# Kernel optimization log

Measured on AMD Instinct MI355X. Metric: run time of the kernel, lower is better.

The kernel has to match this reference:

```python
import jax, jax.numpy as jnp
import numpy as np

B, L, IN_DIM, D_MODEL, N_LAYERS = 4, 1024, 64, 512, 3
D_INNER, STATE, DT_RANK, K = 1024, 16, 32, 4  # expand=2, dt_rank=d_model//16, conv kernel 4


def setup_inputs() -> dict:
    key = jax.random.key(0)
    ks = jax.random.split(key, 8)
    s = 0.02
    def rn(k, shp):
        return jax.random.normal(k, shp, jnp.float32) * s
    inp = {"x": jax.random.normal(ks[0], (B, L, IN_DIM), jnp.float32)}
    inp["input_w"] = rn(ks[1], (D_MODEL, IN_DIM)); inp["input_b"] = jnp.zeros((D_MODEL,), jnp.float32)
    inp["in_proj_w"] = rn(ks[2], (N_LAYERS, 2 * D_INNER, D_MODEL)); inp["in_proj_b"] = jnp.zeros((N_LAYERS, 2 * D_INNER), jnp.float32)
    inp["conv_w"] = rn(ks[3], (N_LAYERS, D_INNER, 1, K)); inp["conv_b"] = jnp.zeros((N_LAYERS, D_INNER), jnp.float32)
    inp["x_proj_w"] = rn(ks[4], (N_LAYERS, DT_RANK + 2 * STATE, D_INNER))
    inp["dt_proj_w"] = rn(ks[5], (N_LAYERS, D_INNER, DT_RANK)); inp["dt_proj_b"] = jnp.full((N_LAYERS, D_INNER), -4.0, jnp.float32)
    inp["A_log"] = jnp.tile(jnp.log(jnp.arange(1, STATE + 1, dtype=jnp.float32))[None, None, :], (N_LAYERS, D_INNER, 1))
    inp["D"] = jnp.ones((N_LAYERS, D_INNER), jnp.float32)
    inp["out_proj_w"] = rn(ks[6], (N_LAYERS, D_MODEL, D_INNER)); inp["out_proj_b"] = jnp.zeros((N_LAYERS, D_MODEL), jnp.float32)
    inp["ln_w"] = jnp.ones((N_LAYERS, D_MODEL), jnp.float32); inp["ln_b"] = jnp.zeros((N_LAYERS, D_MODEL), jnp.float32)
    return inp


def _layernorm(x, w, b):
    mu = jnp.mean(x, -1, keepdims=True)
    v = jnp.var(x, -1, keepdims=True)
    return (x - mu) * jax.lax.rsqrt(v + 1e-5) * w + b


def _mamba(u, iw, ib, cw, cb, xw, dw, db, A_log, Dp, ow, ob):
    # u: [B, L, d_model]
    xz = u @ iw.T + ib                          # [B, L, 2*d_inner]
    xp, z = jnp.split(xz, 2, axis=-1)
    # causal depthwise conv over time
    xc = jax.lax.conv_general_dilated(xp.transpose(0, 2, 1), cw, (1,), [(K - 1, 0)],
                                      feature_group_count=D_INNER,
                                      dimension_numbers=("NCH", "OIH", "NCH")) + cb[None, :, None]
    xc = jax.nn.silu(xc).transpose(0, 2, 1)     # [B, L, d_inner]
    proj = xc @ xw.T                            # [B, L, dt_rank + 2*N]
    dtl = proj[..., :DT_RANK]
    Bm = proj[..., DT_RANK:DT_RANK + STATE]
    Cm = proj[..., DT_RANK + STATE:]
    dt = jax.nn.softplus(dtl @ dw.T + db)       # [B, L, d_inner]
    A = -jnp.exp(A_log)                         # [d_inner, N]

    def step(h, t):
        dt_t, B_t, C_t, x_t = t                 # [B,d], [B,N], [B,N], [B,d]
        h = h * jnp.exp(dt_t[..., None] * A) + (dt_t * x_t)[..., None] * B_t[:, None, :]
        return h, jnp.einsum("bdn,bn->bd", h, C_t)

    h0 = jnp.zeros((u.shape[0], D_INNER, STATE), u.dtype)
    _, ys = jax.lax.scan(step, h0, (dt.transpose(1, 0, 2), Bm.transpose(1, 0, 2),
                                    Cm.transpose(1, 0, 2), xc.transpose(1, 0, 2)))
    y = ys.transpose(1, 0, 2) + xc * Dp
    y = y * jax.nn.silu(z)
    return y @ ow.T + ob


def reference(x, input_w, input_b, in_proj_w, in_proj_b, conv_w, conv_b, x_proj_w,
              dt_proj_w, dt_proj_b, A_log, D, out_proj_w, out_proj_b, ln_w, ln_b):
    h = x @ input_w.T + input_b                 # [B, L, d_model]
    for i in range(N_LAYERS):
        res = h
        h = _mamba(h, in_proj_w[i], in_proj_b[i], conv_w[i], conv_b[i], x_proj_w[i],
                   dt_proj_w[i], dt_proj_b[i], A_log[i], D[i], out_proj_w[i], out_proj_b[i])
        h = _layernorm(h + res, ln_w[i], ln_b[i])
    return h[:, -1, :]
```

## Files before the change

kernel.cpp:

```cpp
#include <hip/hip_runtime.h>
#include <hip/hip_bf16.h>
#include <cstddef>
#include <cstdint>

#define NB 4
#define NL 1024
#define IN_DIM 64
#define D_MODEL 512
#define N_LAYERS 3
#define D_INNER 1024
#define NSTATE 16
#define DT_RANK 32
#define KCONV 4
#define NROWS (NB * NL)
#define CHUNK 16
#define NCHUNK (NL / CHUNK)
#define LOG2E 1.4426950408889634f

typedef __attribute__((ext_vector_type(8))) short short8;
typedef __attribute__((ext_vector_type(4))) float f32x4;
typedef __attribute__((ext_vector_type(4))) unsigned short us4;
typedef unsigned short ushort_t;

__device__ __forceinline__ ushort_t f2b1(float x) {
  uint32_t u = __builtin_bit_cast(uint32_t, x);
  u += 0x7fffu + ((u >> 16) & 1u);
  return (ushort_t)(u >> 16);
}
__device__ __forceinline__ float b2f(ushort_t u) {
  return __builtin_bit_cast(float, (uint32_t)u << 16);
}

__device__ __forceinline__ void gload_lds16(const ushort_t* src, short* dst) {
  __builtin_amdgcn_global_load_lds(
      (const __attribute__((address_space(1))) uint32_t*)src,
      (__attribute__((address_space(3))) uint32_t*)dst, 16, 0, 0);
}

#define E0 (NROWS * IN_DIM)
#define E1 (D_MODEL * IN_DIM)
#define E2 (N_LAYERS * 2 * D_INNER * D_MODEL)
#define E3 (N_LAYERS * 64 * D_INNER)
#define E4 (N_LAYERS * D_INNER * DT_RANK)
#define E5 (N_LAYERS * D_MODEL * D_INNER)
#define ETOT (E0 + E1 + E2 + E3 + E4 + E5)

__global__ __launch_bounds__(256) void cvt_all(
    const float* __restrict__ x, const float* __restrict__ inw,
    const float* __restrict__ ipw, const float* __restrict__ xpw,
    const float* __restrict__ dpw, const float* __restrict__ opw,
    ushort_t* __restrict__ xb, ushort_t* __restrict__ inwb,
    ushort_t* __restrict__ iwb, ushort_t* __restrict__ xwb,
    ushort_t* __restrict__ dwb, ushort_t* __restrict__ owb)
{
  int i = (blockIdx.x * 256 + threadIdx.x) * 4;
  if (i >= ETOT) return;
  const float* src; ushort_t* dst; int off;
  if      (i < E0)                  { src = x;   dst = xb;   off = i; }
  else if (i < E0+E1)               { src = inw; dst = inwb; off = i - E0; }
  else if (i < E0+E1+E2)            { src = ipw; dst = iwb;  off = i - (E0+E1); }
  else if (i < E0+E1+E2+E3)         { src = xpw; dst = xwb;  off = i - (E0+E1+E2); }
  else if (i < E0+E1+E2+E3+E4)      { src = dpw; dst = dwb;  off = i - (E0+E1+E2+E3); }
  else                              { src = opw; dst = owb;  off = i - (E0+E1+E2+E3+E4); }
  const float4 v = *(const float4*)(src + off);
  us4 o;
  o.x = f2b1(v.x); o.y = f2b1(v.y); o.z = f2b1(v.z); o.w = f2b1(v.w);
  *(us4*)(dst + off) = o;
}

template<int BM, int BN, int MF, int NF, int ACT, bool WF32, bool WB16>
__global__ __launch_bounds__(256) void gemm_mfma(
    const ushort_t* __restrict__ A, int lda,
    const ushort_t* __restrict__ W,
    const float* __restrict__ bias,
    float* __restrict__ Cf, ushort_t* __restrict__ Cb,
    int M, int N, int K)
{
  constexpr int CA = BM / 64;
  constexpr int CB = BN / 64;
  __shared__ __align__(16) short sa[BM * 32];
  __shared__ __align__(16) short sb[BN * 32];

  const int tid = threadIdx.x;
  const int l = tid & 63;
  const int wid = tid >> 6;
  const int wrow = (wid >> 1) * (BM / 2);
  const int wcol = (wid & 1) * (BN / 2);
  const int m0 = blockIdx.y * BM;
  const int n0 = blockIdx.x * BN;

  const int srow = l >> 2;
  const int scol = (l & 3) * 8;

  f32x4 acc[MF][NF] = {};

  for (int k0 = 0; k0 < K; k0 += 32) {
#pragma unroll
    for (int c = 0; c < CA; ++c) {
      short* dst = sa + (c * 4 + wid) * 512;
      const ushort_t* src =
          A + (size_t)(m0 + (c * 4 + wid) * 16 + srow) * lda + k0 + scol;
      gload_lds16(src, dst);
    }
#pragma unroll
    for (int c = 0; c < CB; ++c) {
      short* dst = sb + (c * 4 + wid) * 512;
      const ushort_t* src =
          W + (size_t)(n0 + (c * 4 + wid) * 16 + srow) * K + k0 + scol;
      gload_lds16(src, dst);
    }
    __syncthreads();

    short8 af[MF], bfr[NF];
#pragma unroll
    for (int mi = 0; mi < MF; ++mi)
      af[mi] = *(const short8*)(sa + (wrow + mi * 16 + (l & 15)) * 32 + (l >> 4) * 8);
#pragma unroll
    for (int nj = 0; nj < NF; ++nj)
      bfr[nj] = *(const short8*)(sb + (wcol + nj * 16 + (l & 15)) * 32 + (l >> 4) * 8);
#pragma unroll
    for (int mi = 0; mi < MF; ++mi)
#pragma unroll
      for (int nj = 0; nj < NF; ++nj)
        acc[mi][nj] = __builtin_amdgcn_mfma_f32_16x16x32_bf16(
            af[mi], bfr[nj], acc[mi][nj], 0, 0, 0);
    __syncthreads();
  }

#pragma unroll
  for (int nj = 0; nj < NF; ++nj) {
    const int col = n0 + wcol + nj * 16 + (l & 15);
    const float bv = bias ? bias[col] : 0.f;
#pragma unroll
    for (int mi = 0; mi < MF; ++mi) {
#pragma unroll
      for (int q = 0; q < 4; ++q) {
        const int row = m0 + wrow + mi * 16 + (l >> 4) * 4 + q;
        float v = acc[mi][nj][q] + bv;
        if (ACT == 1) v = (v > 20.f) ? v : log1pf(__expf(v));
        if (WF32) Cf[(size_t)row * N + col] = v;
        if (WB16) Cb[(size_t)row * N + col] = f2b1(v);
      }
    }
  }
}

__global__ __launch_bounds__(256) void conv_silu(
    const ushort_t* __restrict__ xzb,
    const float* __restrict__ cw,
    const float* __restrict__ cb,
    ushort_t* __restrict__ xcb)
{
  const int idx = blockIdx.x * 256 + threadIdx.x;
  const int d4 = (idx & (D_INNER / 4 - 1)) * 4;
  const int bt = idx >> 8;
  const int t = bt & (NL - 1);
  const int b = bt >> 10;

  float acc4[4];
  {
    const float4 cbv = *(const float4*)(cb + d4);
    acc4[0] = cbv.x; acc4[1] = cbv.y; acc4[2] = cbv.z; acc4[3] = cbv.w;
  }
  float wv[4][4];
#pragma unroll
  for (int i = 0; i < 4; ++i) {
    const float4 w = *(const float4*)(cw + (size_t)(d4 + i) * KCONV);
    wv[i][0] = w.x; wv[i][1] = w.y; wv[i][2] = w.z; wv[i][3] = w.w;
  }
#pragma unroll
  for (int j = 0; j < KCONV; ++j) {
    const int tt = t - (KCONV - 1) + j;
    if (tt >= 0) {
      const us4 xv = *(const us4*)(xzb + (size_t)(b * NL + tt) * (2 * D_INNER) + d4);
      acc4[0] = fmaf(b2f(xv.x), wv[0][j], acc4[0]);
      acc4[1] = fmaf(b2f(xv.y), wv[1][j], acc4[1]);
      acc4[2] = fmaf(b2f(xv.z), wv[2][j], acc4[2]);
      acc4[3] = fmaf(b2f(xv.w), wv[3][j], acc4[3]);
    }
  }
  us4 o;
#pragma unroll
  for (int i = 0; i < 4; ++i) {
    const float s = acc4[i] / (1.f + __expf(-acc4[i]));
    ((ushort_t*)&o)[i] = f2b1(s);
  }
  *(us4*)(xcb + (size_t)idx * 4) = o;
}

__global__ __launch_bounds__(256) void scan_phase1(
    const ushort_t* __restrict__ dtb,
    const float* __restrict__ proj,
    const ushort_t* __restrict__ xcb,
    const float* __restrict__ A_log,
    float* __restrict__ S_loc,
    float* __restrict__ sumdt)
{
  __shared__ float prs[CHUNK][64];
  const int d = blockIdx.x * 256 + threadIdx.x;
  const int c = blockIdx.y;
  const int b = blockIdx.z;
  const int t0 = c * CHUNK;

#pragma unroll
  for (int i = 0; i < 4; ++i) {
    const int idx = i * 256 + threadIdx.x;
    prs[idx >> 6][idx & 63] =
        proj[((size_t)(b * NL + t0) + (idx >> 6)) * 64 + (idx & 63)];
  }
  __syncthreads();

  float A2[NSTATE];
#pragma unroll
  for (int n = 0; n < NSTATE; ++n)
    A2[n] = -__expf(A_log[d * NSTATE + n]) * LOG2E;

  float h[NSTATE];
#pragma unroll
  for (int n = 0; n < NSTATE; ++n) h[n] = 0.f;
  float sdt = 0.f;

#pragma unroll 4
  for (int tt = 0; tt < CHUNK; ++tt) {
    const size_t row = (size_t)(b * NL + t0 + tt);
    const float dtv = b2f(dtb[row * D_INNER + d]);
    const float xv = b2f(xcb[row * D_INNER + d]);
    float Bv[NSTATE];
    *(float4*)(Bv)      = *(const float4*)(&prs[tt][32]);
    *(float4*)(Bv + 4)  = *(const float4*)(&prs[tt][36]);
    *(float4*)(Bv + 8)  = *(const float4*)(&prs[tt][40]);
    *(float4*)(Bv + 12) = *(const float4*)(&prs[tt][44]);
    sdt += dtv;
    const float dx = dtv * xv;
#pragma unroll
    for (int n = 0; n < NSTATE; ++n)
      h[n] = fmaf(h[n], exp2f(dtv * A2[n]), dx * Bv[n]);
  }

  const size_t cbase = (size_t)(b * NCHUNK + c);
  sumdt[cbase * D_INNER + d] = sdt;
#pragma unroll
  for (int n = 0; n < NSTATE; ++n)
    S_loc[(cbase * NSTATE + n) * D_INNER + d] = h[n];
}

__global__ __launch_bounds__(256) void scan_carry(
    const float* __restrict__ S_loc,
    const float* __restrict__ sumdt,
    const float* __restrict__ A_log,
    float* __restrict__ H_in)
{
  const int idx = blockIdx.x * 256 + threadIdx.x;
  const int d = idx & (D_INNER - 1);
  const int n = (idx >> 10) & (NSTATE - 1);
  const int b = idx >> 14;

  const float A2n = -__expf(A_log[d * NSTATE + n]) * LOG2E;

  float H = 0.f;
  for (int c = 0; c < NCHUNK; ++c) {
    const size_t cbase = (size_t)(b * NCHUNK + c);
    H_in[(cbase * NSTATE + n) * D_INNER + d] = H;
    const float sdt = sumdt[cbase * D_INNER + d];
    H = fmaf(H, exp2f(A2n * sdt), S_loc[(cbase * NSTATE + n) * D_INNER + d]);
  }
}

__global__ __launch_bounds__(256) void scan_phase2(
    const ushort_t* __restrict__ dtb,
    const float* __restrict__ proj,
    const ushort_t* __restrict__ xcb,
    const ushort_t* __restrict__ xzb,
    const float* __restrict__ A_log,
    const float* __restrict__ Dp,
    const float* __restrict__ H_in,
    ushort_t* __restrict__ yb)
{
  __shared__ float prs[CHUNK][64];
  const int d = blockIdx.x * 256 + threadIdx.x;
  const int c = blockIdx.y;
  const int b = blockIdx.z;
  const int t0 = c * CHUNK;

#pragma unroll
  for (int i = 0; i < 4; ++i) {
    const int idx = i * 256 + threadIdx.x;
    prs[idx >> 6][idx & 63] =
        proj[((size_t)(b * NL + t0) + (idx >> 6)) * 64 + (idx & 63)];
  }
  __syncthreads();

  float A2[NSTATE];
#pragma unroll
  for (int n = 0; n < NSTATE; ++n)
    A2[n] = -__expf(A_log[d * NSTATE + n]) * LOG2E;

  const size_t cbase = (size_t)(b * NCHUNK + c);
  float h[NSTATE];
#pragma unroll
  for (int n = 0; n < NSTATE; ++n)
    h[n] = H_in[(cbase * NSTATE + n) * D_INNER + d];

  const float Dv = Dp[d];

#pragma unroll 4
  for (int tt = 0; tt < CHUNK; ++tt) {
    const size_t row = (size_t)(b * NL + t0 + tt);
    const size_t rd = row * D_INNER + d;
    const float dtv = b2f(dtb[rd]);
    const float xv = b2f(xcb[rd]);
    float Bv[NSTATE], Cv[NSTATE];
    *(float4*)(Bv)      = *(const float4*)(&prs[tt][32]);
    *(float4*)(Bv + 4)  = *(const float4*)(&prs[tt][36]);
    *(float4*)(Bv + 8)  = *(const float4*)(&prs[tt][40]);
    *(float4*)(Bv + 12) = *(const float4*)(&prs[tt][44]);
    *(float4*)(Cv)      = *(const float4*)(&prs[tt][48]);
    *(float4*)(Cv + 4)  = *(const float4*)(&prs[tt][52]);
    *(float4*)(Cv + 8)  = *(const float4*)(&prs[tt][56]);
    *(float4*)(Cv + 12) = *(const float4*)(&prs[tt][60]);
    const float dx = dtv * xv;
    float accv = 0.f;
#pragma unroll
    for (int n = 0; n < NSTATE; ++n) {
      h[n] = fmaf(h[n], exp2f(dtv * A2[n]), dx * Bv[n]);
      accv = fmaf(h[n], Cv[n], accv);
    }
    const float zv = b2f(xzb[row * (2 * D_INNER) + D_INNER + d]);
    float yv = fmaf(xv, Dv, accv);
    yv *= zv / (1.f + __expf(-zv));
    yb[rd] = f2b1(yv);
  }
}

__global__ __launch_bounds__(256) void add_ln(
    const float* __restrict__ x,
    const float* __restrict__ res,
    const float* __restrict__ w,
    const float* __restrict__ bln,
    float* __restrict__ out,
    ushort_t* __restrict__ outb,
    float* __restrict__ out2)
{
  const int wave = threadIdx.x >> 6;
  const int lane = threadIdx.x & 63;
  const int row = blockIdx.x * 4 + wave;
  const float* xr = x + (size_t)row * D_MODEL;
  const float* rr = res + (size_t)row * D_MODEL;

  float v[8];
  float s = 0.f, s2 = 0.f;
#pragma unroll
  for (int i = 0; i < 8; ++i) {
    const float t = xr[lane + i * 64] + rr[lane + i * 64];
    v[i] = t; s += t; s2 = fmaf(t, t, s2);
  }
#pragma unroll
  for (int off = 32; off; off >>= 1) {
    s += __shfl_xor(s, off);
    s2 += __shfl_xor(s2, off);
  }
  const float mean = s * (1.f / D_MODEL);
  const float var = s2 * (1.f / D_MODEL) - mean * mean;
  const float rstd = rsqrtf(var + 1e-5f);
  const bool last_t = (row & (NL - 1)) == (NL - 1);
#pragma unroll
  for (int i = 0; i < 8; ++i) {
    const int c = lane + i * 64;
    const float o = (v[i] - mean) * rstd * w[c] + bln[c];
    out[(size_t)row * D_MODEL + c] = o;
    outb[(size_t)row * D_MODEL + c] = f2b1(o);
    if (out2 && last_t) out2[(size_t)(row >> 10) * D_MODEL + c] = o;
  }
}

extern "C" void kernel_launch(void* const* d_in, const int* in_sizes, int n_in,
                              void* d_out, int out_size, void* d_ws, size_t ws_size,
                              hipStream_t stream)
{
  const float* x         = (const float*)d_in[0];
  const float* input_w   = (const float*)d_in[1];
  const float* input_b   = (const float*)d_in[2];
  const float* in_proj_w = (const float*)d_in[3];
  const float* in_proj_b = (const float*)d_in[4];
  const float* conv_w    = (const float*)d_in[5];
  const float* conv_b    = (const float*)d_in[6];
  const float* x_proj_w  = (const float*)d_in[7];
  const float* dt_proj_w = (const float*)d_in[8];
  const float* dt_proj_b = (const float*)d_in[9];
  const float* A_log     = (const float*)d_in[10];
  const float* Dp        = (const float*)d_in[11];
  const float* out_proj_w= (const float*)d_in[12];
  const float* out_proj_b= (const float*)d_in[13];
  const float* ln_w      = (const float*)d_in[14];
  const float* ln_b      = (const float*)d_in[15];

  float* p = (float*)d_ws;
  float* h0   = p; p += (size_t)NROWS * D_MODEL;
  float* h1   = p; p += (size_t)NROWS * D_MODEL;
  float* tmp  = p; p += (size_t)NROWS * D_MODEL;
  float* proj = p; p += (size_t)NROWS * 64;
  float* Sloc = p; p += (size_t)NB * NCHUNK * NSTATE * D_INNER;
  float* Hin  = p; p += (size_t)NB * NCHUNK * NSTATE * D_INNER;
  float* sdt  = p; p += (size_t)NB * NCHUNK * D_INNER;
  ushort_t* q = (ushort_t*)p;
  ushort_t* xzb   = q; q += (size_t)NROWS * 2 * D_INNER;
  ushort_t* xcb   = q; q += (size_t)NROWS * D_INNER;
  ushort_t* dtbb  = q; q += (size_t)NROWS * D_INNER;
  ushort_t* projb = q; q += (size_t)NROWS * 64;
  ushort_t* yb    = q; q += (size_t)NROWS * D_INNER;
  ushort_t* hb    = q; q += (size_t)NROWS * D_MODEL;
  ushort_t* xb    = q; q += (size_t)E0;
  ushort_t* inwb  = q; q += (size_t)E1;
  ushort_t* iwb   = q; q += (size_t)E2;
  ushort_t* xwb   = q; q += (size_t)E3;
  ushort_t* dwb   = q; q += (size_t)E4;
  ushort_t* owb   = q; q += (size_t)E5;

  cvt_all<<<(ETOT / 4 + 255) / 256, 256, 0, stream>>>(
      x, input_w, in_proj_w, x_proj_w, dt_proj_w, out_proj_w,
      xb, inwb, iwb, xwb, dwb, owb);

  gemm_mfma<64, 64, 2, 2, 0, true, true>
      <<<dim3(D_MODEL / 64, NROWS / 64), 256, 0, stream>>>(
      xb, IN_DIM, inwb, input_b, h0, hb, NROWS, D_MODEL, IN_DIM);

  float* hc = h0;
  float* hn = h1;

  for (int l = 0; l < N_LAYERS; ++l) {
    const ushort_t* iw = iwb + (size_t)l * 2 * D_INNER * D_MODEL;
    const float* ib = in_proj_b + (size_t)l * 2 * D_INNER;
    const float* cw = conv_w    + (size_t)l * D_INNER * KCONV;
    const float* cb = conv_b    + (size_t)l * D_INNER;
    const ushort_t* xw = xwb + (size_t)l * 64 * D_INNER;
    const ushort_t* dw = dwb + (size_t)l * D_INNER * DT_RANK;
    const float* db = dt_proj_b + (size_t)l * D_INNER;
    const float* Al = A_log     + (size_t)l * D_INNER * NSTATE;
    const float* Dl = Dp        + (size_t)l * D_INNER;
    const ushort_t* ow = owb + (size_t)l * D_MODEL * D_INNER;
    const float* ob = out_proj_b+ (size_t)l * D_MODEL;
    const float* lw = ln_w      + (size_t)l * D_MODEL;
    const float* lb = ln_b      + (size_t)l * D_MODEL;

    gemm_mfma<128, 128, 4, 4, 0, false, true>
        <<<dim3(2 * D_INNER / 128, NROWS / 128), 256, 0, stream>>>(
        hb, D_MODEL, iw, ib, nullptr, xzb, NROWS, 2 * D_INNER, D_MODEL);

    conv_silu<<<NROWS * D_INNER / 4 / 256, 256, 0, stream>>>(xzb, cw, cb, xcb);

    gemm_mfma<64, 64, 2, 2, 0, true, true>
        <<<dim3(1, NROWS / 64), 256, 0, stream>>>(
        xcb, D_INNER, xw, nullptr, proj, projb, NROWS, 64, D_INNER);

    gemm_mfma<128, 128, 4, 4, 1, false, true>
        <<<dim3(D_INNER / 128, NROWS / 128), 256, 0, stream>>>(
        projb, 64, dw, db, nullptr, dtbb, NROWS, D_INNER, DT_RANK);

    scan_phase1<<<dim3(D_INNER / 256, NCHUNK, NB), 256, 0, stream>>>(
        dtbb, proj, xcb, Al, Sloc, sdt);
    scan_carry<<<(NB * NSTATE * D_INNER) / 256, 256, 0, stream>>>(
        Sloc, sdt, Al, Hin);
    scan_phase2<<<dim3(D_INNER / 256, NCHUNK, NB), 256, 0, stream>>>(
        dtbb, proj, xcb, xzb, Al, Dl, Hin, yb);

    gemm_mfma<128, 128, 4, 4, 0, true, false>
        <<<dim3(D_MODEL / 128, NROWS / 128), 256, 0, stream>>>(
        yb, D_INNER, ow, ob, tmp, nullptr, NROWS, D_MODEL, D_INNER);

    add_ln<<<NROWS / 4, 256, 0, stream>>>(
        tmp, hc, lw, lb, hn, hb,
        (l == N_LAYERS - 1) ? (float*)d_out : nullptr);

    float* t2 = hc; hc = hn; hn = t2;
  }
}
```

Before: 600.3 us.

## Fuse dt projection and softplus into scan kernels, drop dt GEMM

Removes the separate dt_proj GEMM and its bf16 dt buffer. Each scan thread now loads its fp32 dt_proj weight row and computes dt by a 32-term dot product plus softplus from the projection already staged in shared memory. This cuts a kernel launch and the write and double read of a large intermediate, but adds per-timestep ALU work and register pressure in both scan phases. The out_proj GEMM tile is also changed to 64x128 to get more blocks.

```diff
diff --git a/kernel.cpp b/kernel.cpp
--- a/kernel.cpp
+++ b/kernel.cpp
@@ -41,34 +41,32 @@
 #define E1 (D_MODEL * IN_DIM)
 #define E2 (N_LAYERS * 2 * D_INNER * D_MODEL)
 #define E3 (N_LAYERS * 64 * D_INNER)
-#define E4 (N_LAYERS * D_INNER * DT_RANK)
 #define E5 (N_LAYERS * D_MODEL * D_INNER)
-#define ETOT (E0 + E1 + E2 + E3 + E4 + E5)
+#define ETOT (E0 + E1 + E2 + E3 + E5)
 
 __global__ __launch_bounds__(256) void cvt_all(
     const float* __restrict__ x, const float* __restrict__ inw,
     const float* __restrict__ ipw, const float* __restrict__ xpw,
-    const float* __restrict__ dpw, const float* __restrict__ opw,
+    const float* __restrict__ opw,
     ushort_t* __restrict__ xb, ushort_t* __restrict__ inwb,
     ushort_t* __restrict__ iwb, ushort_t* __restrict__ xwb,
-    ushort_t* __restrict__ dwb, ushort_t* __restrict__ owb)
+    ushort_t* __restrict__ owb)
 {
   int i = (blockIdx.x * 256 + threadIdx.x) * 4;
   if (i >= ETOT) return;
   const float* src; ushort_t* dst; int off;
-  if      (i < E0)                  { src = x;   dst = xb;   off = i; }
-  else if (i < E0+E1)               { src = inw; dst = inwb; off = i - E0; }
-  else if (i < E0+E1+E2)            { src = ipw; dst = iwb;  off = i - (E0+E1); }
-  else if (i < E0+E1+E2+E3)         { src = xpw; dst = xwb;  off = i - (E0+E1+E2); }
-  else if (i < E0+E1+E2+E3+E4)      { src = dpw; dst = dwb;  off = i - (E0+E1+E2+E3); }
-  else                              { src = opw; dst = owb;  off = i - (E0+E1+E2+E3+E4); }
+  if      (i < E0)            { src = x;   dst = xb;   off = i; }
+  else if (i < E0+E1)         { src = inw; dst = inwb; off = i - E0; }
+  else if (i < E0+E1+E2)      { src = ipw; dst = iwb;  off = i - (E0+E1); }
+  else if (i < E0+E1+E2+E3)   { src = xpw; dst = xwb;  off = i - (E0+E1+E2); }
+  else                        { src = opw; dst = owb;  off = i - (E0+E1+E2+E3); }
   const float4 v = *(const float4*)(src + off);
   us4 o;
   o.x = f2b1(v.x); o.y = f2b1(v.y); o.z = f2b1(v.z); o.w = f2b1(v.w);
   *(us4*)(dst + off) = o;
 }
 
-template<int BM, int BN, int MF, int NF, int ACT, bool WF32, bool WB16>
+template<int BM, int BN, int MF, int NF, bool WF32, bool WB16>
 __global__ __launch_bounds__(256) void gemm_mfma(
     const ushort_t* __restrict__ A, int lda,
     const ushort_t* __restrict__ W,
@@ -137,7 +135,6 @@
       for (int q = 0; q < 4; ++q) {
         const int row = m0 + wrow + mi * 16 + (l >> 4) * 4 + q;
         float v = acc[mi][nj][q] + bv;
-        if (ACT == 1) v = (v > 20.f) ? v : log1pf(__expf(v));
         if (WF32) Cf[(size_t)row * N + col] = v;
         if (WB16) Cb[(size_t)row * N + col] = f2b1(v);
       }
@@ -188,11 +185,31 @@
   *(us4*)(xcb + (size_t)idx * 4) = o;
 }
 
+__device__ __forceinline__ void load_dw_row(
+    const float* __restrict__ dpw, int d, float* dwr, float& dbv,
+    const float* __restrict__ db)
+{
+#pragma unroll
+  for (int i = 0; i < 8; ++i)
+    *(float4*)(dwr + i * 4) = *(const float4*)(dpw + (size_t)d * DT_RANK + i * 4);
+  dbv = db[d];
+}
+
+__device__ __forceinline__ float dt_fused(
+    const float* __restrict__ dtl, const float* __restrict__ dwr, float dbv)
+{
+  float a = dbv;
+#pragma unroll
+  for (int j = 0; j < DT_RANK; ++j) a = fmaf(dtl[j], dwr[j], a);
+  return (a > 20.f) ? a : log1pf(__expf(a));
+}
+
 __global__ __launch_bounds__(256) void scan_phase1(
-    const ushort_t* __restrict__ dtb,
     const float* __restrict__ proj,
     const ushort_t* __restrict__ xcb,
     const float* __restrict__ A_log,
+    const float* __restrict__ dpw,
+    const float* __restrict__ db,
     float* __restrict__ S_loc,
     float* __restrict__ sumdt)
 {
@@ -210,6 +227,9 @@
   }
   __syncthreads();
 
+  float dwr[DT_RANK]; float dbv;
+  load_dw_row(dpw, d, dwr, dbv, db);
+
   float A2[NSTATE];
 #pragma unroll
   for (int n = 0; n < NSTATE; ++n)
@@ -220,10 +240,9 @@
   for (int n = 0; n < NSTATE; ++n) h[n] = 0.f;
   float sdt = 0.f;
 
-#pragma unroll 4
   for (int tt = 0; tt < CHUNK; ++tt) {
     const size_t row = (size_t)(b * NL + t0 + tt);
-    const float dtv = b2f(dtb[row * D_INNER + d]);
+    const float dtv = dt_fused(&prs[tt][0], dwr, dbv);
     const float xv = b2f(xcb[row * D_INNER + d]);
     float Bv[NSTATE];
     *(float4*)(Bv)      = *(const float4*)(&prs[tt][32]);
@@ -267,11 +286,12 @@
 }
 
 __global__ __launch_bounds__(256) void scan_phase2(
-    const ushort_t* __restrict__ dtb,
     const float* __restrict__ proj,
     const ushort_t* __restrict__ xcb,
     const ushort_t* __restrict__ xzb,
     const float* __restrict__ A_log,
+    const float* __restrict__ dpw,
+    const float* __restrict__ db,
     const float* __restrict__ Dp,
     const float* __restrict__ H_in,
     ushort_t* __restrict__ yb)
@@ -290,6 +310,9 @@
   }
   __syncthreads();
 
+  float dwr[DT_RANK]; float dbv;
+  load_dw_row(dpw, d, dwr, dbv, db);
+
   float A2[NSTATE];
 #pragma unroll
   for (int n = 0; n < NSTATE; ++n)
@@ -303,11 +326,10 @@
 
   const float Dv = Dp[d];
 
-#pragma unroll 4
   for (int tt = 0; tt < CHUNK; ++tt) {
     const size_t row = (size_t)(b * NL + t0 + tt);
     const size_t rd = row * D_INNER + d;
-    const float dtv = b2f(dtb[rd]);
+    const float dtv = dt_fused(&prs[tt][0], dwr, dbv);
     const float xv = b2f(xcb[rd]);
     float Bv[NSTATE], Cv[NSTATE];
     *(float4*)(Bv)      = *(const float4*)(&prs[tt][32]);
@@ -405,22 +427,19 @@
   ushort_t* q = (ushort_t*)p;
   ushort_t* xzb   = q; q += (size_t)NROWS * 2 * D_INNER;
   ushort_t* xcb   = q; q += (size_t)NROWS * D_INNER;
-  ushort_t* dtbb  = q; q += (size_t)NROWS * D_INNER;
-  ushort_t* projb = q; q += (size_t)NROWS * 64;
   ushort_t* yb    = q; q += (size_t)NROWS * D_INNER;
   ushort_t* hb    = q; q += (size_t)NROWS * D_MODEL;
   ushort_t* xb    = q; q += (size_t)E0;
   ushort_t* inwb  = q; q += (size_t)E1;
   ushort_t* iwb   = q; q += (size_t)E2;
   ushort_t* xwb   = q; q += (size_t)E3;
-  ushort_t* dwb   = q; q += (size_t)E4;
   ushort_t* owb   = q; q += (size_t)E5;
 
   cvt_all<<<(ETOT / 4 + 255) / 256, 256, 0, stream>>>(
-      x, input_w, in_proj_w, x_proj_w, dt_proj_w, out_proj_w,
-      xb, inwb, iwb, xwb, dwb, owb);
-
-  gemm_mfma<64, 64, 2, 2, 0, true, true>
+      x, input_w, in_proj_w, x_proj_w, out_proj_w,
+      xb, inwb, iwb, xwb, owb);
+
+  gemm_mfma<64, 64, 2, 2, true, true>
       <<<dim3(D_MODEL / 64, NROWS / 64), 256, 0, stream>>>(
       xb, IN_DIM, inwb, input_b, h0, hb, NROWS, D_MODEL, IN_DIM);
 
@@ -433,7 +452,7 @@
     const float* cw = conv_w    + (size_t)l * D_INNER * KCONV;
     const float* cb = conv_b    + (size_t)l * D_INNER;
     const ushort_t* xw = xwb + (size_t)l * 64 * D_INNER;
-    const ushort_t* dw = dwb + (size_t)l * D_INNER * DT_RANK;
+    const float* dwf = dt_proj_w + (size_t)l * D_INNER * DT_RANK;
     const float* db = dt_proj_b + (size_t)l * D_INNER;
     const float* Al = A_log     + (size_t)l * D_INNER * NSTATE;
     const float* Dl = Dp        + (size_t)l * D_INNER;
@@ -442,29 +461,25 @@
     const float* lw = ln_w      + (size_t)l * D_MODEL;
     const float* lb = ln_b      + (size_t)l * D_MODEL;
 
-    gemm_mfma<128, 128, 4, 4, 0, false, true>
+    gemm_mfma<128, 128, 4, 4, false, true>
         <<<dim3(2 * D_INNER / 128, NROWS / 128), 256, 0, stream>>>(
         hb, D_MODEL, iw, ib, nullptr, xzb, NROWS, 2 * D_INNER, D_MODEL);
 
     conv_silu<<<NROWS * D_INNER / 4 / 256, 256, 0, stream>>>(xzb, cw, cb, xcb);
 
-    gemm_mfma<64, 64, 2, 2, 0, true, true>
+    gemm_mfma<64, 64, 2, 2, true, false>
         <<<dim3(1, NROWS / 64), 256, 0, stream>>>(
-        xcb, D_INNER, xw, nullptr, proj, projb, NROWS, 64, D_INNER);
-
-    gemm_mfma<128, 128, 4, 4, 1, false, true>
-        <<<dim3(D_INNER / 128, NROWS / 128), 256, 0, stream>>>(
-        projb, 64, dw, db, nullptr, dtbb, NROWS, D_INNER, DT_RANK);
+        xcb, D_INNER, xw, nullptr, proj, nullptr, NROWS, 64, D_INNER);
 
     scan_phase1<<<dim3(D_INNER / 256, NCHUNK, NB), 256, 0, stream>>>(
-        dtbb, proj, xcb, Al, Sloc, sdt);
+        proj, xcb, Al, dwf, db, Sloc, sdt);
     scan_carry<<<(NB * NSTATE * D_INNER) / 256, 256, 0, stream>>>(
         Sloc, sdt, Al, Hin);
     scan_phase2<<<dim3(D_INNER / 256, NCHUNK, NB), 256, 0, stream>>>(
-        dtbb, proj, xcb, xzb, Al, Dl, Hin, yb);
-
-    gemm_mfma<128, 128, 4, 4, 0, true, false>
-        <<<dim3(D_MODEL / 128, NROWS / 128), 256, 0, stream>>>(
+        proj, xcb, xzb, Al, dwf, db, Dl, Hin, yb);
+
+    gemm_mfma<64, 128, 2, 4, true, false>
+        <<<dim3(D_MODEL / 128, NROWS / 64), 256, 0, stream>>>(
         yb, D_INNER, ow, ob, tmp, nullptr, NROWS, D_MODEL, D_INNER);
 
     add_ln<<<NROWS / 4, 256, 0, stream>>>(
```

Measured after the change: 608.3 us. Within noise of the previous version (+1.3%).
